# Optimization experiments

Hardware: AMD Instinct MI355X
Metric: run time of the kernel (lower is better)

The kernel has to match this reference:

```python
import jax, jax.numpy as jnp
import numpy as np

N = 20000          # num nodes
E_EDGES = 160000   # num edges
D = 128            # input feature dim
H = 128            # hidden dim
C = 128            # num_classes (expert output dim)
NE = 4             # num_experts
COEF = 0.01        # load-balancing loss coefficient


def setup_inputs() -> dict:
    key = jax.random.key(0)
    ks = jax.random.split(key, 8)
    x = jax.random.normal(ks[0], (N, D), jnp.float32)
    edge_index = jax.random.randint(ks[1], (2, E_EDGES), 0, N)
    x_agg = jax.random.normal(ks[2], (N, D), jnp.float32)
    # gate params (w_gate is zeros-init in source; use small randn so gating is exercised)
    w_gate = jax.random.normal(ks[3], (D, NE), jnp.float32) * 0.1
    gate_threshold = jax.random.normal(ks[4], (NE,), jnp.float32) * 0.1
    experts_mask = jnp.ones((NE,), jnp.float32)
    # per-expert 2-layer GCN weights (vectorized over expert dim)
    W1 = jax.random.normal(ks[5], (NE, D, H), jnp.float32) * (1.0 / np.sqrt(D))
    b1 = jnp.zeros((NE, H), jnp.float32)
    W2 = jax.random.normal(ks[6], (NE, H, C), jnp.float32) * (1.0 / np.sqrt(H))
    b2 = jnp.zeros((NE, C), jnp.float32)
    return {"x": x, "edge_index": edge_index, "x_agg": x_agg,
            "w_gate": w_gate, "gate_threshold": gate_threshold,
            "experts_mask": experts_mask, "W1": W1, "b1": b1, "W2": W2, "b2": b2}


def _gcn_norm(edge_index):
    src, dst = edge_index[0], edge_index[1]
    deg = jax.ops.segment_sum(jnp.ones((src.shape[0],), jnp.float32), dst, num_segments=N)
    deg = jnp.maximum(deg, 1.0)
    norm = jax.lax.rsqrt(deg[src] * deg[dst])  # symmetric GCN normalization per edge
    return src, dst, norm


def _agg(h, src, dst, norm):
    # h: [N, F] -> normalized neighbor sum: [N, F]
    return jax.ops.segment_sum(h[src] * norm[:, None], dst, num_segments=N)


def _ste_sign(s):
    # SAGMMGateBackward: sign in forward, identity in backward (straight-through)
    return s + jax.lax.stop_gradient(jnp.sign(s) - s)


def reference(x, edge_index, x_agg, w_gate, gate_threshold, experts_mask, W1, b1, W2, b2):
    src, dst, norm = _gcn_norm(edge_index)

    # --- noisy_top_any gating (eval path: no noise), add_sigmoid=True ---
    clean_logits = x_agg @ w_gate                       # [N, NE]
    gate_scores = jax.nn.sigmoid(clean_logits)          # [N, NE]
    # sign-based straight-through gate vs learned threshold, masked by experts_mask
    gates = jax.nn.relu(_ste_sign(gate_scores - gate_threshold[None, :]))
    gates = gates * experts_mask[None, :]               # [N, NE], binary in forward

    # --- experts: 4 two-layer GCNs, vectorized over the expert dim ---
    agg_x = _agg(x, src, dst, norm)                     # shared first aggregation [N, D]
    h = jax.nn.relu(jnp.einsum('nd,edh->enh', agg_x, W1) + b1[:, None, :])   # [NE, N, H]
    agg_h = jax.vmap(lambda hh: _agg(hh, src, dst, norm))(h)                 # [NE, N, H]
    expert_out = jnp.einsum('enh,ehc->enc', agg_h, W2) + b2[:, None, :]      # [NE, N, C]

    # --- combine expert outputs with gates ---
    output = jnp.einsum('ne,enc->nc', gates, expert_out)                     # [N, C]

    # --- cv_squared load-balancing loss on per-expert importance ---
    importance = gates.sum(axis=0)                                           # [NE]
    load_loss = COEF * (jnp.var(importance) / (jnp.mean(importance) ** 2 + 1e-10))
    return output, load_loss
```

## Files before the change

### kernel.cpp

```cpp
#include <hip/hip_runtime.h>
#include <cstdint>
#include <cstddef>

#define NNODES 20000
#define NEDGES 160000
#define DFEAT  128
#define NEXP   4

typedef unsigned short u16;
typedef __attribute__((ext_vector_type(8))) short short8v;
typedef __attribute__((ext_vector_type(4))) float float4v;

static __device__ __forceinline__ u16 f2bf(float f) {
    union { float f; unsigned int i; } v; v.f = f;
    unsigned int r = (v.i + 0x7FFFu + ((v.i >> 16) & 1u)) >> 16;
    return (u16)r;
}
static __device__ __forceinline__ unsigned pack2(float a, float b) {
    return ((unsigned)f2bf(b) << 16) | f2bf(a);
}
static __device__ __forceinline__ float lo2f(unsigned int u) { return __uint_as_float(u << 16); }
static __device__ __forceinline__ float hi2f(unsigned int u) { return __uint_as_float(u & 0xFFFF0000u); }

static __device__ __forceinline__ void acc8(float w, uint4 v, float* a) {
    a[0] += w * lo2f(v.x); a[1] += w * hi2f(v.x);
    a[2] += w * lo2f(v.y); a[3] += w * hi2f(v.y);
    a[4] += w * lo2f(v.z); a[5] += w * hi2f(v.z);
    a[6] += w * lo2f(v.w); a[7] += w * hi2f(v.w);
}


__global__ void k_pre(const int* __restrict__ ei, const float* __restrict__ x,
                      const float* __restrict__ W1, const float* __restrict__ W2,
                      const float* __restrict__ x_agg, const float* __restrict__ w_gate,
                      const float* __restrict__ thr, const float* __restrict__ mask,
                      float* __restrict__ deg, u16* __restrict__ W1t, u16* __restrict__ W2t,
                      float* __restrict__ gates, float* __restrict__ importance,
                      u16* __restrict__ xbf) {
    int b = blockIdx.x;
    if (b < 625) {
        int e = b * 256 + threadIdx.x;
        if (e < NEDGES) atomicAdd(&deg[ei[NEDGES + e]], 1.0f);
        return;
    }
    if (b < 753) {
        __shared__ u16 tile[32][33];
        int tb = b - 625;
        int arr = tb >> 6;
        int t6 = tb & 63;
        int e  = t6 >> 4;
        int kt = (t6 >> 2) & 3;
        int ct = t6 & 3;
        const float* W = arr ? W2 : W1;
        u16* Wt = arr ? W2t : W1t;
        int ty = threadIdx.x >> 5, tx = threadIdx.x & 31;
#pragma unroll
        for (int r = 0; r < 4; ++r) {
            int k = kt * 32 + ty + r * 8;
            int c = ct * 32 + tx;
            tile[ty + r * 8][tx] = f2bf(W[(size_t)e * 16384 + (size_t)k * 128 + c]);
        }
        __syncthreads();
#pragma unroll
        for (int r = 0; r < 4; ++r) {
            int c = ct * 32 + ty + r * 8;
            int k = kt * 32 + tx;
            Wt[(size_t)e * 16384 + (size_t)c * 128 + k] = tile[tx][ty + r * 8];
        }
        return;
    }
    if (b < 832) {
        int n = (b - 753) * 256 + threadIdx.x;
        float4 lg = make_float4(0.f, 0.f, 0.f, 0.f);
        if (n < NNODES) {
            const float4* xr = (const float4*)(x_agg + (size_t)n * DFEAT);
            const float4* wg = (const float4*)w_gate;
            for (int k4 = 0; k4 < 32; ++k4) {
                float4 xv = xr[k4];
                float4 w0 = wg[4 * k4 + 0], w1 = wg[4 * k4 + 1];
                float4 w2 = wg[4 * k4 + 2], w3 = wg[4 * k4 + 3];
                lg.x += xv.x * w0.x + xv.y * w1.x + xv.z * w2.x + xv.w * w3.x;
                lg.y += xv.x * w0.y + xv.y * w1.y + xv.z * w2.y + xv.w * w3.y;
                lg.z += xv.x * w0.z + xv.y * w1.z + xv.z * w2.z + xv.w * w3.z;
                lg.w += xv.x * w0.w + xv.y * w1.w + xv.z * w2.w + xv.w * w3.w;
            }
        }
        float g[4];
        float lv[4] = {lg.x, lg.y, lg.z, lg.w};
        for (int e = 0; e < 4; ++e) {
            float sgm = 1.0f / (1.0f + expf(-lv[e]));
            g[e] = (sgm - thr[e] > 0.0f) ? mask[e] : 0.0f;
            if (n >= NNODES) g[e] = 0.0f;
        }
        if (n < NNODES) ((float4*)gates)[n] = make_float4(g[0], g[1], g[2], g[3]);
        int lane = threadIdx.x & 63;
        for (int e = 0; e < 4; ++e) {
            float v = g[e];
            for (int off = 32; off >= 1; off >>= 1) v += __shfl_down(v, off);
            if (lane == 0) atomicAdd(&importance[e], v);
        }
        return;
    }
    int t8 = (b - 832) * 256 + threadIdx.x;
    const float4* xr = (const float4*)x + (size_t)t8 * 2;
    float4 v0 = xr[0], v1 = xr[1];
    uint4 o;
    o.x = pack2(v0.x, v0.y); o.y = pack2(v0.z, v0.w);
    o.z = pack2(v1.x, v1.y); o.w = pack2(v1.z, v1.w);
    ((uint4*)xbf)[t8] = o;
}

__global__ void k_scan(const float* __restrict__ deg, int* __restrict__ rowstart) {
    __shared__ int part[1024];
    int t = threadIdx.x;
    const int PER = 20;
    int base = t * PER;
    int s = 0;
    for (int i = 0; i < PER; ++i) {
        int n = base + i;
        if (n < NNODES) s += (int)deg[n];
    }
    part[t] = s;
    __syncthreads();
    for (int off = 1; off < 1024; off <<= 1) {
        int v = (t >= off) ? part[t - off] : 0;
        __syncthreads();
        part[t] += v;
        __syncthreads();
    }
    int run = part[t] - s;
    for (int i = 0; i < PER; ++i) {
        int n = base + i;
        if (n < NNODES) {
            rowstart[n] = run;
            run += (int)deg[n];
        }
    }
    if (t == 1023) rowstart[NNODES] = part[1023];
}

__global__ void k_fill(const int* __restrict__ ei, const float* __restrict__ deg,
                       const int* __restrict__ rowstart, int* __restrict__ cursor,
                       int* __restrict__ csrc, float* __restrict__ cnrm) {
    int e = blockIdx.x * 256 + threadIdx.x;
    if (e >= NEDGES) return;
    int s = ei[e], d = ei[NEDGES + e];
    int pos = atomicAdd(&cursor[d], 1);
    int slot = rowstart[d] + pos;
    csrc[slot] = s;
    float ds = fmaxf(deg[s], 1.0f), dd = fmaxf(deg[d], 1.0f);
    cnrm[slot] = 1.0f / sqrtf(ds * dd);
}

__global__ void k_aggx(const u16* __restrict__ xbf, const int* __restrict__ rowstart,
                       const int* __restrict__ csrc, const float* __restrict__ cnrm,
                       u16* __restrict__ aggx) {
    int gid = blockIdx.x * 256 + threadIdx.x;
    if (gid >= NNODES * 16) return;
    int l8 = gid & 15, node = gid >> 4;
    int r0 = rowstart[node], r1 = rowstart[node + 1];
    float a[8] = {0.f, 0.f, 0.f, 0.f, 0.f, 0.f, 0.f, 0.f};
    int j = r0;
    for (; j + 4 <= r1; j += 4) {
        int s0 = csrc[j], s1 = csrc[j + 1], s2 = csrc[j + 2], s3 = csrc[j + 3];
        float w0 = cnrm[j], w1 = cnrm[j + 1], w2 = cnrm[j + 2], w3 = cnrm[j + 3];
        uint4 v0 = ((const uint4*)(xbf + (size_t)s0 * DFEAT))[l8];
        uint4 v1 = ((const uint4*)(xbf + (size_t)s1 * DFEAT))[l8];
        uint4 v2 = ((const uint4*)(xbf + (size_t)s2 * DFEAT))[l8];
        uint4 v3 = ((const uint4*)(xbf + (size_t)s3 * DFEAT))[l8];
        acc8(w0, v0, a); acc8(w1, v1, a); acc8(w2, v2, a); acc8(w3, v3, a);
    }
    for (; j < r1; ++j) {
        int s = csrc[j];
        float w = cnrm[j];
        uint4 v = ((const uint4*)(xbf + (size_t)s * DFEAT))[l8];
        acc8(w, v, a);
    }
    uint4 o;
    o.x = pack2(a[0], a[1]); o.y = pack2(a[2], a[3]);
    o.z = pack2(a[4], a[5]); o.w = pack2(a[6], a[7]);
    ((uint4*)(aggx + (size_t)node * DFEAT))[l8] = o;
}

__launch_bounds__(320)
__global__ void k_gemm1(const u16* __restrict__ aggx, const u16* __restrict__ W1t,
                        const float* __restrict__ b1, u16* __restrict__ h) {
    int e = blockIdx.y;
    int w = threadIdx.x >> 6, l = threadIdx.x & 63;
    int rbase = blockIdx.x * 80 + w * 16;
    int lr = l & 15, kg = l >> 4;

    const short8v* A8 = (const short8v*)aggx;
    const short8v* B8 = (const short8v*)(W1t + (size_t)e * 16384);

    short8v a[4];
#pragma unroll
    for (int kk = 0; kk < 4; ++kk) a[kk] = A8[(size_t)(rbase + lr) * 16 + kk * 4 + kg];

    u16* hb = h + (size_t)e * NNODES * DFEAT;
#pragma unroll
    for (int c = 0; c < 8; ++c) {
        float4v acc = {0.f, 0.f, 0.f, 0.f};
#pragma unroll
        for (int kk = 0; kk < 4; ++kk) {
            short8v b = B8[(c * 16 + lr) * 16 + kk * 4 + kg];
            acc = __builtin_amdgcn_mfma_f32_16x16x32_bf16(a[kk], b, acc, 0, 0, 0);
        }
        float bv = b1[e * DFEAT + c * 16 + lr];
#pragma unroll
        for (int i = 0; i < 4; ++i) {
            int node = rbase + kg * 4 + i;
            float vv = fmaxf(acc[i] + bv, 0.f);
            hb[(size_t)node * DFEAT + c * 16 + lr] = f2bf(vv);
        }
    }
}

__global__ void k_aggh(const u16* __restrict__ h, const int* __restrict__ rowstart,
                       const int* __restrict__ csrc, const float* __restrict__ cnrm,
                       const float* __restrict__ gates, u16* __restrict__ aggh) {
    int gid = blockIdx.x * 256 + threadIdx.x;
    if (gid >= NEXP * NNODES * 16) return;
    int l8 = gid & 15;
    int ni = gid >> 4;
    int node = ni % NNODES;
    int e = ni / NNODES;
    if (gates[(size_t)node * 4 + e] == 0.0f) return;
    const u16* hb = h + (size_t)e * NNODES * DFEAT;
    int r0 = rowstart[node], r1 = rowstart[node + 1];
    float a[8] = {0.f, 0.f, 0.f, 0.f, 0.f, 0.f, 0.f, 0.f};
    int j = r0;
    for (; j + 4 <= r1; j += 4) {
        int s0 = csrc[j], s1 = csrc[j + 1], s2 = csrc[j + 2], s3 = csrc[j + 3];
        float w0 = cnrm[j], w1 = cnrm[j + 1], w2 = cnrm[j + 2], w3 = cnrm[j + 3];
        uint4 v0 = ((const uint4*)(hb + (size_t)s0 * DFEAT))[l8];
        uint4 v1 = ((const uint4*)(hb + (size_t)s1 * DFEAT))[l8];
        uint4 v2 = ((const uint4*)(hb + (size_t)s2 * DFEAT))[l8];
        uint4 v3 = ((const uint4*)(hb + (size_t)s3 * DFEAT))[l8];
        acc8(w0, v0, a); acc8(w1, v1, a); acc8(w2, v2, a); acc8(w3, v3, a);
    }
    for (; j < r1; ++j) {
        int s = csrc[j];
        float w = cnrm[j];
        uint4 v = ((const uint4*)(hb + (size_t)s * DFEAT))[l8];
        acc8(w, v, a);
    }
    uint4 o;
    o.x = pack2(a[0], a[1]); o.y = pack2(a[2], a[3]);
    o.z = pack2(a[4], a[5]); o.w = pack2(a[6], a[7]);
    ((uint4*)(aggh + (size_t)ni * DFEAT))[l8] = o;
}

__launch_bounds__(320)
__global__ void k_gemm2(const u16* __restrict__ aggh, const u16* __restrict__ W2t,
                        const float* __restrict__ b2, const float* __restrict__ gates,
                        const float* __restrict__ importance, float* __restrict__ out) {
    if (blockIdx.x == 0 && blockIdx.y == 0 && threadIdx.x == 0) {
        float v0 = importance[0], v1 = importance[1], v2 = importance[2], v3 = importance[3];
        float mean = 0.25f * (v0 + v1 + v2 + v3);
        float d0 = v0 - mean, d1 = v1 - mean, d2 = v2 - mean, d3 = v3 - mean;
        float var = 0.25f * (d0 * d0 + d1 * d1 + d2 * d2 + d3 * d3);
        out[(size_t)NNODES * DFEAT] = 0.01f * var / (mean * mean + 1e-10f);
    }
    int w = threadIdx.x >> 6, l = threadIdx.x & 63;
    int rbase = blockIdx.x * 80 + w * 16;
    int cb = blockIdx.y * 2;
    int lr = l & 15, kg = l >> 4;

    float4v acc[2];
    acc[0] = (float4v){0.f, 0.f, 0.f, 0.f};
    acc[1] = (float4v){0.f, 0.f, 0.f, 0.f};

#pragma unroll
    for (int e = 0; e < NEXP; ++e) {
        const short8v* A8 = (const short8v*)(aggh + (size_t)e * NNODES * DFEAT);
        const short8v* B8 = (const short8v*)(W2t + (size_t)e * 16384);
        short8v a[4];
#pragma unroll
        for (int kk = 0; kk < 4; ++kk) a[kk] = A8[(size_t)(rbase + lr) * 16 + kk * 4 + kg];
        float g[4];
#pragma unroll
        for (int i = 0; i < 4; ++i) g[i] = gates[(size_t)(rbase + kg * 4 + i) * 4 + e];
#pragma unroll
        for (int c = 0; c < 2; ++c) {
            float4v t = {0.f, 0.f, 0.f, 0.f};
#pragma unroll
            for (int kk = 0; kk < 4; ++kk) {
                short8v b = B8[((cb + c) * 16 + lr) * 16 + kk * 4 + kg];
                t = __builtin_amdgcn_mfma_f32_16x16x32_bf16(a[kk], b, t, 0, 0, 0);
            }
            float bv = b2[e * DFEAT + (cb + c) * 16 + lr];
#pragma unroll
            for (int i = 0; i < 4; ++i) acc[c][i] += g[i] * (t[i] + bv);
        }
    }

#pragma unroll
    for (int c = 0; c < 2; ++c)
#pragma unroll
        for (int i = 0; i < 4; ++i) {
            int node = rbase + kg * 4 + i;
            out[(size_t)node * DFEAT + (cb + c) * 16 + lr] = acc[c][i];
        }
}

extern "C" void kernel_launch(void* const* d_in, const int* in_sizes, int n_in,
                              void* d_out, int out_size, void* d_ws, size_t ws_size,
                              hipStream_t stream) {
    const float* x      = (const float*)d_in[0];
    const int*   ei     = (const int*)d_in[1];
    const float* x_agg  = (const float*)d_in[2];
    const float* w_gate = (const float*)d_in[3];
    const float* thr    = (const float*)d_in[4];
    const float* mask   = (const float*)d_in[5];
    const float* W1     = (const float*)d_in[6];
    const float* b1     = (const float*)d_in[7];
    const float* W2     = (const float*)d_in[8];
    const float* b2     = (const float*)d_in[9];
    float* out = (float*)d_out;
    float* ws  = (float*)d_ws;

    float* deg        = ws;
    int*   cursor     = (int*)(ws + 20000);
    float* importance = ws + 40000;
    int*   rowstart   = (int*)(ws + 40960);
    int*   csrc       = (int*)(ws + 61440);
    float* cnrm       = ws + 221440;
    float* gates      = ws + 381440;
    u16*   W1t        = (u16*)(ws + 461440);
    u16*   W2t        = (u16*)(ws + 494208);
    u16*   xbf        = (u16*)(ws + 526976);
    u16*   aggx       = (u16*)(ws + 1806976);
    u16*   h          = (u16*)(ws + 3086976);
    u16*   aggh       = (u16*)(ws + 8206976);

    hipMemsetAsync(d_ws, 0, 40008 * sizeof(float), stream);

    k_pre<<<2082, 256, 0, stream>>>(ei, x, W1, W2, x_agg, w_gate, thr, mask,
                                    deg, W1t, W2t, gates, importance, xbf);
    k_scan<<<1, 1024, 0, stream>>>(deg, rowstart);
    k_fill<<<(NEDGES + 255) / 256, 256, 0, stream>>>(ei, deg, rowstart, cursor, csrc, cnrm);
    k_aggx<<<(NNODES * 16) / 256, 256, 0, stream>>>(xbf, rowstart, csrc, cnrm, aggx);
    k_gemm1<<<dim3(250, NEXP), 320, 0, stream>>>(aggx, W1t, b1, h);
    k_aggh<<<(NEXP * NNODES * 16) / 256, 256, 0, stream>>>(h, rowstart, csrc, cnrm, gates, aggh);
    k_gemm2<<<dim3(250, 4), 320, 0, stream>>>(aggh, W2t, b2, gates, importance, out);
}
```

Before: 242.5 us.

## Fuse neighbor aggregation into GEMM kernels via shared-memory staging

Merges the first aggregation with the first expert GEMM, and the second aggregation with the gated second GEMM. Each block aggregates 80 nodes into LDS and then runs MFMA on them, so the aggx and aggh intermediates are never written to or read from global memory, and two launches are dropped. In exchange the grid shrinks to 250 blocks, which may underfill the GPU and reduce latency hiding for the irregular gathers. The second kernel also serializes the four experts inside each block, with barriers between aggregation and GEMM.

```diff
diff --git a/kernel.cpp b/kernel.cpp
--- a/kernel.cpp
+++ b/kernel.cpp
@@ -152,155 +152,155 @@
     cnrm[slot] = 1.0f / sqrtf(ds * dd);
 }
 
-__global__ void k_aggx(const u16* __restrict__ xbf, const int* __restrict__ rowstart,
-                       const int* __restrict__ csrc, const float* __restrict__ cnrm,
-                       u16* __restrict__ aggx) {
-    int gid = blockIdx.x * 256 + threadIdx.x;
-    if (gid >= NNODES * 16) return;
-    int l8 = gid & 15, node = gid >> 4;
-    int r0 = rowstart[node], r1 = rowstart[node + 1];
-    float a[8] = {0.f, 0.f, 0.f, 0.f, 0.f, 0.f, 0.f, 0.f};
-    int j = r0;
-    for (; j + 4 <= r1; j += 4) {
-        int s0 = csrc[j], s1 = csrc[j + 1], s2 = csrc[j + 2], s3 = csrc[j + 3];
-        float w0 = cnrm[j], w1 = cnrm[j + 1], w2 = cnrm[j + 2], w3 = cnrm[j + 3];
-        uint4 v0 = ((const uint4*)(xbf + (size_t)s0 * DFEAT))[l8];
-        uint4 v1 = ((const uint4*)(xbf + (size_t)s1 * DFEAT))[l8];
-        uint4 v2 = ((const uint4*)(xbf + (size_t)s2 * DFEAT))[l8];
-        uint4 v3 = ((const uint4*)(xbf + (size_t)s3 * DFEAT))[l8];
-        acc8(w0, v0, a); acc8(w1, v1, a); acc8(w2, v2, a); acc8(w3, v3, a);
-    }
-    for (; j < r1; ++j) {
-        int s = csrc[j];
-        float w = cnrm[j];
-        uint4 v = ((const uint4*)(xbf + (size_t)s * DFEAT))[l8];
-        acc8(w, v, a);
-    }
-    uint4 o;
-    o.x = pack2(a[0], a[1]); o.y = pack2(a[2], a[3]);
-    o.z = pack2(a[4], a[5]); o.w = pack2(a[6], a[7]);
-    ((uint4*)(aggx + (size_t)node * DFEAT))[l8] = o;
-}
-
 __launch_bounds__(320)
-__global__ void k_gemm1(const u16* __restrict__ aggx, const u16* __restrict__ W1t,
-                        const float* __restrict__ b1, u16* __restrict__ h) {
-    int e = blockIdx.y;
-    int w = threadIdx.x >> 6, l = threadIdx.x & 63;
-    int rbase = blockIdx.x * 80 + w * 16;
+__global__ void k_ag1(const u16* __restrict__ xbf, const int* __restrict__ rowstart,
+                      const int* __restrict__ csrc, const float* __restrict__ cnrm,
+                      const u16* __restrict__ W1t, const float* __restrict__ b1,
+                      u16* __restrict__ h) {
+    __shared__ uint4 As[80 * 17];
+    int t = threadIdx.x;
+    int nbase = blockIdx.x * 80;
+
+    for (int it = t; it < 1280; it += 320) {
+        int nl = it >> 4, l8 = it & 15;
+        int node = nbase + nl;
+        int r0 = rowstart[node], r1 = rowstart[node + 1];
+        float a[8] = {0.f, 0.f, 0.f, 0.f, 0.f, 0.f, 0.f, 0.f};
+        int j = r0;
+        for (; j + 4 <= r1; j += 4) {
+            int s0 = csrc[j], s1 = csrc[j + 1], s2 = csrc[j + 2], s3 = csrc[j + 3];
+            float w0 = cnrm[j], w1 = cnrm[j + 1], w2 = cnrm[j + 2], w3 = cnrm[j + 3];
+            uint4 v0 = ((const uint4*)(xbf + (size_t)s0 * DFEAT))[l8];
+            uint4 v1 = ((const uint4*)(xbf + (size_t)s1 * DFEAT))[l8];
+            uint4 v2 = ((const uint4*)(xbf + (size_t)s2 * DFEAT))[l8];
+            uint4 v3 = ((const uint4*)(xbf + (size_t)s3 * DFEAT))[l8];
+            acc8(w0, v0, a); acc8(w1, v1, a); acc8(w2, v2, a); acc8(w3, v3, a);
+        }
+        for (; j < r1; ++j) {
+            uint4 v = ((const uint4*)(xbf + (size_t)csrc[j] * DFEAT))[l8];
+            acc8(cnrm[j], v, a);
+        }
+        uint4 o;
+        o.x = pack2(a[0], a[1]); o.y = pack2(a[2], a[3]);
+        o.z = pack2(a[4], a[5]); o.w = pack2(a[6], a[7]);
+        As[nl * 17 + l8] = o;
+    }
+    __syncthreads();
+
+    int w = t >> 6, l = t & 63;
     int lr = l & 15, kg = l >> 4;
-
-    const short8v* A8 = (const short8v*)aggx;
-    const short8v* B8 = (const short8v*)(W1t + (size_t)e * 16384);
-
+    const short8v* As8 = (const short8v*)As;
     short8v a[4];
 #pragma unroll
-    for (int kk = 0; kk < 4; ++kk) a[kk] = A8[(size_t)(rbase + lr) * 16 + kk * 4 + kg];
-
-    u16* hb = h + (size_t)e * NNODES * DFEAT;
-#pragma unroll
-    for (int c = 0; c < 8; ++c) {
-        float4v acc = {0.f, 0.f, 0.f, 0.f};
-#pragma unroll
-        for (int kk = 0; kk < 4; ++kk) {
-            short8v b = B8[(c * 16 + lr) * 16 + kk * 4 + kg];
-            acc = __builtin_amdgcn_mfma_f32_16x16x32_bf16(a[kk], b, acc, 0, 0, 0);
-        }
-        float bv = b1[e * DFEAT + c * 16 + lr];
-#pragma unroll
-        for (int i = 0; i < 4; ++i) {
-            int node = rbase + kg * 4 + i;
-            float vv = fmaxf(acc[i] + bv, 0.f);
-            hb[(size_t)node * DFEAT + c * 16 + lr] = f2bf(vv);
-        }
-    }
-}
-
-__global__ void k_aggh(const u16* __restrict__ h, const int* __restrict__ rowstart,
-                       const int* __restrict__ csrc, const float* __restrict__ cnrm,
-                       const float* __restrict__ gates, u16* __restrict__ aggh) {
-    int gid = blockIdx.x * 256 + threadIdx.x;
-    if (gid >= NEXP * NNODES * 16) return;
-    int l8 = gid & 15;
-    int ni = gid >> 4;
-    int node = ni % NNODES;
-    int e = ni / NNODES;
-    if (gates[(size_t)node * 4 + e] == 0.0f) return;
-    const u16* hb = h + (size_t)e * NNODES * DFEAT;
-    int r0 = rowstart[node], r1 = rowstart[node + 1];
-    float a[8] = {0.f, 0.f, 0.f, 0.f, 0.f, 0.f, 0.f, 0.f};
-    int j = r0;
-    for (; j + 4 <= r1; j += 4) {
-        int s0 = csrc[j], s1 = csrc[j + 1], s2 = csrc[j + 2], s3 = csrc[j + 3];
-        float w0 = cnrm[j], w1 = cnrm[j + 1], w2 = cnrm[j + 2], w3 = cnrm[j + 3];
-        uint4 v0 = ((const uint4*)(hb + (size_t)s0 * DFEAT))[l8];
-        uint4 v1 = ((const uint4*)(hb + (size_t)s1 * DFEAT))[l8];
-        uint4 v2 = ((const uint4*)(hb + (size_t)s2 * DFEAT))[l8];
-        uint4 v3 = ((const uint4*)(hb + (size_t)s3 * DFEAT))[l8];
-        acc8(w0, v0, a); acc8(w1, v1, a); acc8(w2, v2, a); acc8(w3, v3, a);
-    }
-    for (; j < r1; ++j) {
-        int s = csrc[j];
-        float w = cnrm[j];
-        uint4 v = ((const uint4*)(hb + (size_t)s * DFEAT))[l8];
-        acc8(w, v, a);
-    }
-    uint4 o;
-    o.x = pack2(a[0], a[1]); o.y = pack2(a[2], a[3]);
-    o.z = pack2(a[4], a[5]); o.w = pack2(a[6], a[7]);
-    ((uint4*)(aggh + (size_t)ni * DFEAT))[l8] = o;
+    for (int kk = 0; kk < 4; ++kk) a[kk] = As8[(w * 16 + lr) * 17 + kk * 4 + kg];
+
+#pragma unroll
+    for (int e = 0; e < NEXP; ++e) {
+        const short8v* B8 = (const short8v*)(W1t + (size_t)e * 16384);
+        u16* hb = h + (size_t)e * NNODES * DFEAT;
+#pragma unroll
+        for (int c = 0; c < 8; ++c) {
+            float4v acc = {0.f, 0.f, 0.f, 0.f};
+#pragma unroll
+            for (int kk = 0; kk < 4; ++kk) {
+                short8v bfr = B8[(c * 16 + lr) * 16 + kk * 4 + kg];
+                acc = __builtin_amdgcn_mfma_f32_16x16x32_bf16(a[kk], bfr, acc, 0, 0, 0);
+            }
+            float bv = b1[e * DFEAT + c * 16 + lr];
+#pragma unroll
+            for (int i = 0; i < 4; ++i) {
+                int node = nbase + w * 16 + kg * 4 + i;
+                float vv = fmaxf(acc[i] + bv, 0.f);
+                hb[(size_t)node * DFEAT + c * 16 + lr] = f2bf(vv);
+            }
+        }
+    }
 }
 
 __launch_bounds__(320)
-__global__ void k_gemm2(const u16* __restrict__ aggh, const u16* __restrict__ W2t,
-                        const float* __restrict__ b2, const float* __restrict__ gates,
-                        const float* __restrict__ importance, float* __restrict__ out) {
-    if (blockIdx.x == 0 && blockIdx.y == 0 && threadIdx.x == 0) {
+__global__ void k_ag2(const u16* __restrict__ h, const int* __restrict__ rowstart,
+                      const int* __restrict__ csrc, const float* __restrict__ cnrm,
+                      const u16* __restrict__ W2t, const float* __restrict__ b2,
+                      const float* __restrict__ gates, const float* __restrict__ importance,
+                      float* __restrict__ out) {
+    if (blockIdx.x == 0 && threadIdx.x == 0) {
         float v0 = importance[0], v1 = importance[1], v2 = importance[2], v3 = importance[3];
         float mean = 0.25f * (v0 + v1 + v2 + v3);
         float d0 = v0 - mean, d1 = v1 - mean, d2 = v2 - mean, d3 = v3 - mean;
         float var = 0.25f * (d0 * d0 + d1 * d1 + d2 * d2 + d3 * d3);
         out[(size_t)NNODES * DFEAT] = 0.01f * var / (mean * mean + 1e-10f);
     }
-    int w = threadIdx.x >> 6, l = threadIdx.x & 63;
-    int rbase = blockIdx.x * 80 + w * 16;
-    int cb = blockIdx.y * 2;
+    __shared__ uint4 As[80 * 17];
+    int t = threadIdx.x;
+    int nbase = blockIdx.x * 80;
+    int w = t >> 6, l = t & 63;
     int lr = l & 15, kg = l >> 4;
-
-    float4v acc[2];
-    acc[0] = (float4v){0.f, 0.f, 0.f, 0.f};
-    acc[1] = (float4v){0.f, 0.f, 0.f, 0.f};
-
-#pragma unroll
+    const short8v* As8 = (const short8v*)As;
+
+    float4v acc[8];
+#pragma unroll
+    for (int c = 0; c < 8; ++c) acc[c] = (float4v){0.f, 0.f, 0.f, 0.f};
+
+    float gw[4];
+
     for (int e = 0; e < NEXP; ++e) {
-        const short8v* A8 = (const short8v*)(aggh + (size_t)e * NNODES * DFEAT);
+        __syncthreads();
+        const u16* hb = h + (size_t)e * NNODES * DFEAT;
+        for (int it = t; it < 1280; it += 320) {
+            int nl = it >> 4, l8 = it & 15;
+            int node = nbase + nl;
+            uint4 o = make_uint4(0u, 0u, 0u, 0u);
+            if (gates[(size_t)node * 4 + e] != 0.0f) {
+                int r0 = rowstart[node], r1 = rowstart[node + 1];
+                float a[8] = {0.f, 0.f, 0.f, 0.f, 0.f, 0.f, 0.f, 0.f};
+                int j = r0;
+                for (; j + 4 <= r1; j += 4) {
+                    int s0 = csrc[j], s1 = csrc[j + 1], s2 = csrc[j + 2], s3 = csrc[j + 3];
+                    float w0 = cnrm[j], w1 = cnrm[j + 1], w2 = cnrm[j + 2], w3 = cnrm[j + 3];
+                    uint4 v0 = ((const uint4*)(hb + (size_t)s0 * DFEAT))[l8];
+                    uint4 v1 = ((const uint4*)(hb + (size_t)s1 * DFEAT))[l8];
+                    uint4 v2 = ((const uint4*)(hb + (size_t)s2 * DFEAT))[l8];
+                    uint4 v3 = ((const uint4*)(hb + (size_t)s3 * DFEAT))[l8];
+                    acc8(w0, v0, a); acc8(w1, v1, a); acc8(w2, v2, a); acc8(w3, v3, a);
+                }
+                for (; j < r1; ++j) {
+                    uint4 v = ((const uint4*)(hb + (size_t)csrc[j] * DFEAT))[l8];
+                    acc8(cnrm[j], v, a);
+                }
+                o.x = pack2(a[0], a[1]); o.y = pack2(a[2], a[3]);
+                o.z = pack2(a[4], a[5]); o.w = pack2(a[6], a[7]);
+            }
+            As[nl * 17 + l8] = o;
+        }
+        __syncthreads();
+
+        short8v a[4];
+#pragma unroll
+        for (int kk = 0; kk < 4; ++kk) a[kk] = As8[(w * 16 + lr) * 17 + kk * 4 + kg];
+#pragma unroll
+        for (int i = 0; i < 4; ++i)
+            gw[i] = gates[(size_t)(nbase + w * 16 + kg * 4 + i) * 4 + e];
         const short8v* B8 = (const short8v*)(W2t + (size_t)e * 16384);
-        short8v a[4];
-#pragma unroll
-        for (int kk = 0; kk < 4; ++kk) a[kk] = A8[(size_t)(rbase + lr) * 16 + kk * 4 + kg];
-        float g[4];
-#pragma unroll
-        for (int i = 0; i < 4; ++i) g[i] = gates[(size_t)(rbase + kg * 4 + i) * 4 + e];
-#pragma unroll
-        for (int c = 0; c < 2; ++c) {
-            float4v t = {0.f, 0.f, 0.f, 0.f};
+#pragma unroll
+        for (int c = 0; c < 8; ++c) {
+            float4v tv = {0.f, 0.f, 0.f, 0.f};
 #pragma unroll
             for (int kk = 0; kk < 4; ++kk) {
-                short8v b = B8[((cb + c) * 16 + lr) * 16 + kk * 4 + kg];
-                t = __builtin_amdgcn_mfma_f32_16x16x32_bf16(a[kk], b, t, 0, 0, 0);
-            }
-            float bv = b2[e * DFEAT + (cb + c) * 16 + lr];
-#pragma unroll
-            for (int i = 0; i < 4; ++i) acc[c][i] += g[i] * (t[i] + bv);
-        }
-    }
-
-#pragma unroll
-    for (int c = 0; c < 2; ++c)
+                short8v bfr = B8[(c * 16 + lr) * 16 + kk * 4 + kg];
+                tv = __builtin_amdgcn_mfma_f32_16x16x32_bf16(a[kk], bfr, tv, 0, 0, 0);
+            }
+            float bv = b2[e * DFEAT + c * 16 + lr];
+#pragma unroll
+            for (int i = 0; i < 4; ++i) acc[c][i] += gw[i] * (tv[i] + bv);
+        }
+    }
+
+#pragma unroll
+    for (int c = 0; c < 8; ++c)
 #pragma unroll
         for (int i = 0; i < 4; ++i) {
-            int node = rbase + kg * 4 + i;
-            out[(size_t)node * DFEAT + (cb + c) * 16 + lr] = acc[c][i];
+            int node = nbase + w * 16 + kg * 4 + i;
+            out[(size_t)node * DFEAT + c * 16 + lr] = acc[c][i];
         }
 }
 
@@ -330,9 +330,7 @@
     u16*   W1t        = (u16*)(ws + 461440);
     u16*   W2t        = (u16*)(ws + 494208);
     u16*   xbf        = (u16*)(ws + 526976);
-    u16*   aggx       = (u16*)(ws + 1806976);
-    u16*   h          = (u16*)(ws + 3086976);
-    u16*   aggh       = (u16*)(ws + 8206976);
+    u16*   h          = (u16*)(ws + 1806976);
 
     hipMemsetAsync(d_ws, 0, 40008 * sizeof(float), stream);
 
@@ -340,8 +338,6 @@
                                     deg, W1t, W2t, gates, importance, xbf);
     k_scan<<<1, 1024, 0, stream>>>(deg, rowstart);
     k_fill<<<(NEDGES + 255) / 256, 256, 0, stream>>>(ei, deg, rowstart, cursor, csrc, cnrm);
-    k_aggx<<<(NNODES * 16) / 256, 256, 0, stream>>>(xbf, rowstart, csrc, cnrm, aggx);
-    k_gemm1<<<dim3(250, NEXP), 320, 0, stream>>>(aggx, W1t, b1, h);
-    k_aggh<<<(NEXP * NNODES * 16) / 256, 256, 0, stream>>>(h, rowstart, csrc, cnrm, gates, aggh);
-    k_gemm2<<<dim3(250, 4), 320, 0, stream>>>(aggh, W2t, b2, gates, importance, out);
-}
+    k_ag1<<<250, 320, 0, stream>>>(xbf, rowstart, csrc, cnrm, W1t, b1, h);
+    k_ag2<<<250, 320, 0, stream>>>(h, rowstart, csrc, cnrm, W2t, b2, gates, importance, out);
+}
```

Result: slower. 284.1 us (+17.1%).
